# Kernel optimization log

Hardware: AMD Instinct MI355X
Metric: run time of the kernel (lower is better)

The kernel has to match this reference:

```python
import jax, jax.numpy as jnp
import numpy as np

L = 8192   # residues / nodes
E = 524288 # contact-map edges (avg degree 64)
NEG_SLOPE = 0.2  # PyG GATConv default negative_slope


def gat_layer(x, src, dst, Wg, asrc, adst, bias):
    """PyG-style GATConv (v1), concat heads, eval mode (no dropout).
    x: [L, F_in]; Wg: [F_in, H*C]; asrc/adst: [H, C]; bias: [H*C]."""
    H, C = asrc.shape
    h = (x @ Wg).reshape(L, H, C)                      # [L,H,C]
    a_s = jnp.einsum('nhc,hc->nh', h, asrc)            # [L,H]
    a_d = jnp.einsum('nhc,hc->nh', h, adst)            # [L,H]
    e = jax.nn.leaky_relu(a_s[src] + a_d[dst], NEG_SLOPE)  # [E',H]
    # softmax over incoming edges of each destination node
    m = jax.ops.segment_max(e, dst, num_segments=L)
    ex = jnp.exp(e - m[dst])
    denom = jax.ops.segment_sum(ex, dst, num_segments=L)
    alpha = ex / (denom[dst] + 1e-16)                  # [E',H]
    msg = h[src] * alpha[:, :, None]                   # [E',H,C]
    out = jax.ops.segment_sum(msg, dst, num_segments=L)  # [L,H,C]
    return out.reshape(L, H * C) + bias


def setup_inputs() -> dict:
    key = jax.random.key(0)
    ks = jax.random.split(key, 16)
    def g(k, shape, scale=0.05):
        return (jax.random.normal(k, shape, dtype=jnp.float32) * scale)
    return {
        'input_seq': jax.random.normal(ks[0], (1, L, 26), dtype=jnp.float32),
        'edge_index': jax.random.randint(ks[1], (2, E), 0, L, dtype=jnp.int32),
        'W1': g(ks[2], (26, 1024)),
        'W2': g(ks[3], (1024, 256)),
        'Wg1': g(ks[4], (256, 256)),
        'asrc1': g(ks[5], (4, 64)),
        'adst1': g(ks[6], (4, 64)),
        'b1': g(ks[7], (256,)),
        'Wg2': g(ks[8], (256, 512)),
        'asrc2': g(ks[9], (4, 128)),
        'adst2': g(ks[10], (4, 128)),
        'b2': g(ks[11], (512,)),
        'fcW': g(ks[12], (512, 512)),
        'fcb': g(ks[13], (512,)),
        'outW': g(ks[14], (512, 489)),
        'outb': g(ks[15], (489,)),
    }


def reference(input_seq, edge_index, W1, W2, Wg1, asrc1, adst1, b1,
              Wg2, asrc2, adst2, b2, fcW, fcb, outW, outb):
    # input_layer: Linear(26,1024,no bias) -> ReLU -> Linear(1024,256,no bias)
    x = jax.nn.relu(input_seq[0] @ W1) @ W2            # [L,256]
    # add self-loops (PyG GATConv default)
    loops = jnp.arange(L, dtype=edge_index.dtype)
    src = jnp.concatenate([edge_index[0], loops])
    dst = jnp.concatenate([edge_index[1], loops])
    # two GAT layers with ReLU activation
    x = jax.nn.relu(gat_layer(x, src, dst, Wg1, asrc1, adst1, b1))  # [L,256]
    x = jax.nn.relu(gat_layer(x, src, dst, Wg2, asrc2, adst2, b2))  # [L,512]
    # sum-pool over residues (x.sum(dim=1) with batch=1)
    pooled = x.sum(axis=0, keepdims=True)              # [1,512]
    # fc layers (dropout inactive in eval)
    h = jax.nn.relu(pooled @ fcW + fcb)                # [1,512]
    return h @ outW + outb                             # [1,489]
```

## Files before the change

### kernel.cpp

```cpp
#include <hip/hip_runtime.h>
#include <hip/hip_bf16.h>

constexpr int L = 8192;
constexpr int H = 4;

typedef __attribute__((ext_vector_type(8))) short bf16x8;
typedef __attribute__((ext_vector_type(8))) unsigned short u16x8;
typedef __attribute__((ext_vector_type(4))) float f32x4;

#if defined(__has_builtin)
#  if __has_builtin(__builtin_amdgcn_fdot2_f32_bf16)
#    define HAVE_DOT2 1
#  endif
#endif
#ifndef HAVE_DOT2
#  define HAVE_DOT2 0
#endif
#if HAVE_DOT2
typedef __attribute__((ext_vector_type(2))) __bf16 bfx2;
#endif

static __device__ __forceinline__ float lrelu(float e) {
  return e > 0.f ? e : 0.2f * e;
}
static __device__ __forceinline__ float b2f(unsigned short s) {
  return __uint_as_float(((unsigned)s) << 16);
}
static __device__ __forceinline__ unsigned short f2b(float f) {
  __hip_bfloat16 h = __float2bfloat16(f);
  return *reinterpret_cast<unsigned short*>(&h);
}
static __device__ __forceinline__ float dot2a(unsigned hv, unsigned m, float acc) {
#if HAVE_DOT2
  return __builtin_amdgcn_fdot2_f32_bf16(
      __builtin_bit_cast(bfx2, hv), __builtin_bit_cast(bfx2, m), acc, false);
#else
  return acc + b2f((unsigned short)(hv & 0xffffu)) * b2f((unsigned short)(m & 0xffffu))
             + b2f((unsigned short)(hv >> 16)) * b2f((unsigned short)(m >> 16));
#endif
}

__global__ __launch_bounds__(256) void conv_combo(
    const float* __restrict__ seq, const float* __restrict__ W1,
    const float* __restrict__ W2, const float* __restrict__ Wg1,
    const float* __restrict__ Wg2, const float* __restrict__ fcW,
    const float* __restrict__ outW, const int* __restrict__ ei,
    const float* __restrict__ as1, const float* __restrict__ ad1,
    const float* __restrict__ as2, const float* __restrict__ ad2,
    int E, int Etot,
    __hip_bfloat16* __restrict__ xb, __hip_bfloat16* __restrict__ W1t,
    __hip_bfloat16* __restrict__ W2t, __hip_bfloat16* __restrict__ Wg1t,
    __hip_bfloat16* __restrict__ Wg2t, float* __restrict__ fcWt,
    float* __restrict__ outWt, float* __restrict__ wa2,
    int* __restrict__ deg, int* __restrict__ rank) {
  __shared__ float tile[32][33];
  int t = threadIdx.x;
  if (blockIdx.x < 992) {
    int b = blockIdx.x;
    const float* src; void* dst; bool obf16; int K, N, Kout, kt, nt;
    if (b < 256)               { src = W2;  dst = W2t;  obf16 = true;  K = 1024; N = 256; Kout = 1024; nt = b & 7;  kt = b >> 3; }
    else if ((b -= 256) < 64)  { src = Wg1; dst = Wg1t; obf16 = true;  K = 256;  N = 256; Kout = 256;  nt = b & 7;  kt = b >> 3; }
    else if ((b -= 64) < 128)  { src = Wg2; dst = Wg2t; obf16 = true;  K = 256;  N = 512; Kout = 256;  nt = b & 15; kt = b >> 4; }
    else if ((b -= 128) < 256) { src = fcW; dst = fcWt; obf16 = false; K = 512;  N = 512; Kout = 512;  nt = b & 15; kt = b >> 4; }
    else if ((b -= 256) < 256) { src = outW;dst = outWt;obf16 = false; K = 512;  N = 489; Kout = 512;  nt = b & 15; kt = b >> 4; }
    else { b -= 256;             src = W1;  dst = W1t;  obf16 = true;  K = 26;   N = 1024;Kout = 32;   nt = b;      kt = 0; }
    int lr = t >> 3, lc4 = (t & 7) * 4;
    int gk = kt * 32 + lr, gn = nt * 32 + lc4;
    float4 v = {0.f, 0.f, 0.f, 0.f};
    if (gk < K) {
      const float* p = &src[(size_t)gk * N + gn];
      v.x = (gn + 0 < N) ? p[0] : 0.f;
      v.y = (gn + 1 < N) ? p[1] : 0.f;
      v.z = (gn + 2 < N) ? p[2] : 0.f;
      v.w = (gn + 3 < N) ? p[3] : 0.f;
    }
    tile[lr][lc4 + 0] = v.x; tile[lr][lc4 + 1] = v.y;
    tile[lr][lc4 + 2] = v.z; tile[lr][lc4 + 3] = v.w;
    __syncthreads();
    int on = nt * 32 + lr, ok = kt * 32 + lc4;
    if (on >= N || ok >= Kout) return;
    float o0 = tile[lc4 + 0][lr], o1 = tile[lc4 + 1][lr];
    float o2 = tile[lc4 + 2][lr], o3 = tile[lc4 + 3][lr];
    if (obf16) {
      ushort4 u = {f2b(o0), f2b(o1), f2b(o2), f2b(o3)};
      *(ushort4*)&((__hip_bfloat16*)dst)[(size_t)on * Kout + ok] = u;
    } else {
      float4 u = {o0, o1, o2, o3};
      *(float4*)&((float*)dst)[(size_t)on * Kout + ok] = u;
    }
    return;
  }
  int bb = blockIdx.x - 992;
  if (bb < 1024) {
    int i = bb * 256 + t;
    int r = i >> 5, k = i & 31;
    xb[i] = __float2bfloat16(k < 26 ? seq[r * 26 + k] : 0.f);
    return;
  }
  bb -= 1024;
  int lane = t & 63, wid = t >> 6;
  if (bb < 512) {
    int idx = bb * 4 + wid;
    int k = idx >> 3, o = idx & 7, h = o & 3;
    const float* av = (o < 4) ? as1 : ad1;
    float v = Wg1[k * 256 + h * 64 + lane] * av[h * 64 + lane];
#pragma unroll
    for (int off = 32; off > 0; off >>= 1) v += __shfl_xor(v, off);
    if (lane == 0) Wg1t[(size_t)(256 + o) * 256 + k] = __float2bfloat16(v);
    return;
  }
  bb -= 512;
  if (bb < 512) {
    int idx = bb * 4 + wid;
    int k = idx >> 3, o = idx & 7, h = o & 3;
    const float* av = (o < 4) ? as2 : ad2;
    float v = Wg2[k * 512 + h * 128 + lane] * av[h * 128 + lane]
            + Wg2[k * 512 + h * 128 + 64 + lane] * av[h * 128 + 64 + lane];
#pragma unroll
    for (int off = 32; off > 0; off >>= 1) v += __shfl_xor(v, off);
    if (lane == 0) wa2[idx] = v;
    return;
  }
  bb -= 512;
  if (bb < 56) {
    int i = bb * 256 + t;
    ((__hip_bfloat16*)Wg1t)[(size_t)264 * 256 + i] = __float2bfloat16(0.f);
    return;
  }
  bb -= 56;
  int e = bb * 256 + t;
  if (e < Etot) {
    int dst = (e < E) ? ei[E + e] : (e - E);
    rank[e] = atomicAdd(&deg[dst], 1);
  }
}

template<int BK, bool RELU, bool ASD>
__global__ __launch_bounds__(256) void gemm_big(
    const __hip_bfloat16* __restrict__ A, const __hip_bfloat16* __restrict__ Bt,
    __hip_bfloat16* __restrict__ C, float* __restrict__ asd,
    int M, int N, int K) {
  __shared__ __align__(16) short As[128][BK + 8];
  __shared__ __align__(16) short Bs[64][BK + 8];
  int tid = threadIdx.x;
  int m0 = blockIdx.y * 128, n0 = blockIdx.x * 64;
  int w = tid >> 6, lane = tid & 63;
  int wm = (w >> 1) * 64, wn = (w & 1) * 32;
  f32x4 acc[4][2] = {};
  for (int k0 = 0; k0 < K; k0 += BK) {
    if constexpr (BK == 64) {
#pragma unroll
      for (int i = 0; i < 4; i++) {
        int ch = i * 256 + tid; int r = ch >> 3, kg = ch & 7;
        *(bf16x8*)&As[r][kg * 8] = *(const bf16x8*)&A[(size_t)(m0 + r) * K + k0 + kg * 8];
      }
#pragma unroll
      for (int i = 0; i < 2; i++) {
        int ch = i * 256 + tid; int r = ch >> 3, kg = ch & 7;
        *(bf16x8*)&Bs[r][kg * 8] = *(const bf16x8*)&Bt[(size_t)(n0 + r) * K + k0 + kg * 8];
      }
    } else {
#pragma unroll
      for (int i = 0; i < 2; i++) {
        int ch = i * 256 + tid; int r = ch >> 2, kg = ch & 3;
        *(bf16x8*)&As[r][kg * 8] = *(const bf16x8*)&A[(size_t)(m0 + r) * K + k0 + kg * 8];
      }
      { int r = tid >> 2, kg = tid & 3;
        *(bf16x8*)&Bs[r][kg * 8] = *(const bf16x8*)&Bt[(size_t)(n0 + r) * K + k0 + kg * 8]; }
    }
    __syncthreads();
    int kk = (lane >> 4) * 8;
#pragma unroll
    for (int ks = 0; ks < BK / 32; ks++) {
      bf16x8 af[4], bfr[2];
#pragma unroll
      for (int m = 0; m < 4; m++)
        af[m] = *(const bf16x8*)&As[wm + m * 16 + (lane & 15)][ks * 32 + kk];
#pragma unroll
      for (int n = 0; n < 2; n++)
        bfr[n] = *(const bf16x8*)&Bs[wn + n * 16 + (lane & 15)][ks * 32 + kk];
#pragma unroll
      for (int m = 0; m < 4; m++)
#pragma unroll
        for (int n = 0; n < 2; n++)
          acc[m][n] = __builtin_amdgcn_mfma_f32_16x16x32_bf16(af[m], bfr[n], acc[m][n], 0, 0, 0);
    }
    __syncthreads();
  }
#pragma unroll
  for (int m = 0; m < 4; m++) {
#pragma unroll
    for (int n = 0; n < 2; n++) {
      int col = n0 + wn + n * 16 + (lane & 15);
#pragma unroll
      for (int j = 0; j < 4; j++) {
        int row = m0 + wm + m * 16 + (lane >> 4) * 4 + j;
        float v = acc[m][n][j];
        if (RELU) v = fmaxf(v, 0.f);
        if (!ASD) {
          C[(size_t)row * N + col] = __float2bfloat16(v);
        } else {
          if (col < N) C[(size_t)row * N + col] = __float2bfloat16(v);
          else if (col < N + 8) asd[(size_t)row * 8 + (col - N)] = v;
        }
      }
    }
  }
}

__global__ __launch_bounds__(256) void gemm_head(
    const __hip_bfloat16* __restrict__ agg,
    const __hip_bfloat16* __restrict__ Wg2t,
    const float* __restrict__ b2,
    float* __restrict__ pooled) {
  constexpr int BK = 64;
  __shared__ __align__(16) short As[128][BK + 8];
  __shared__ __align__(16) short Bs[64][BK + 8];
  __shared__ float s_cs[4][32];
  int tid = threadIdx.x;
  int z = blockIdx.z;
  int m0 = blockIdx.y * 128, n0 = blockIdx.x * 64;
  const __hip_bfloat16* A = agg + (size_t)z * 256;
  const __hip_bfloat16* Bt = Wg2t + (size_t)z * 128 * 256;
  int w = tid >> 6, lane = tid & 63;
  int wm = (w >> 1) * 64, wn = (w & 1) * 32;
  f32x4 acc[4][2] = {};
  for (int k0 = 0; k0 < 256; k0 += BK) {
#pragma unroll
    for (int i = 0; i < 4; i++) {
      int ch = i * 256 + tid; int r = ch >> 3, kg = ch & 7;
      *(bf16x8*)&As[r][kg * 8] = *(const bf16x8*)&A[(size_t)(m0 + r) * 1024 + k0 + kg * 8];
    }
#pragma unroll
    for (int i = 0; i < 2; i++) {
      int ch = i * 256 + tid; int r = ch >> 3, kg = ch & 7;
      *(bf16x8*)&Bs[r][kg * 8] = *(const bf16x8*)&Bt[(size_t)(n0 + r) * 256 + k0 + kg * 8];
    }
    __syncthreads();
    int kk = (lane >> 4) * 8;
#pragma unroll
    for (int ks = 0; ks < BK / 32; ks++) {
      bf16x8 af[4], bfr[2];
#pragma unroll
      for (int m = 0; m < 4; m++)
        af[m] = *(const bf16x8*)&As[wm + m * 16 + (lane & 15)][ks * 32 + kk];
#pragma unroll
      for (int n = 0; n < 2; n++)
        bfr[n] = *(const bf16x8*)&Bs[wn + n * 16 + (lane & 15)][ks * 32 + kk];
#pragma unroll
      for (int m = 0; m < 4; m++)
#pragma unroll
        for (int n = 0; n < 2; n++)
          acc[m][n] = __builtin_amdgcn_mfma_f32_16x16x32_bf16(af[m], bfr[n], acc[m][n], 0, 0, 0);
    }
    __syncthreads();
  }
  float cs[2] = {0.f, 0.f};
#pragma unroll
  for (int n = 0; n < 2; n++) {
    float bv = b2[z * 128 + n0 + wn + n * 16 + (lane & 15)];
#pragma unroll
    for (int m = 0; m < 4; m++)
#pragma unroll
      for (int j = 0; j < 4; j++)
        cs[n] += fmaxf(acc[m][n][j] + bv, 0.f);
  }
#pragma unroll
  for (int n = 0; n < 2; n++) {
    cs[n] += __shfl_xor(cs[n], 16);
    cs[n] += __shfl_xor(cs[n], 32);
  }
  if (lane < 16) { s_cs[w][lane] = cs[0]; s_cs[w][16 + lane] = cs[1]; }
  __syncthreads();
  if (tid < 64) {
    int c = tid;
    int bsel = c >> 5;
    float s = s_cs[bsel][c & 31] + s_cs[bsel + 2][c & 31];
    atomicAdd(&pooled[z * 128 + n0 + c], s);
  }
}

__global__ __launch_bounds__(1024) void scan_deg(const int* __restrict__ deg,
                                                 int* __restrict__ row_start,
                                                 float* __restrict__ pooled) {
  __shared__ int wsum[16];
  int t = threadIdx.x;
  if (t < 512) pooled[t] = 0.f;
  int lane = t & 63, w = t >> 6;
  int local[8];
  int sum = 0;
#pragma unroll
  for (int j = 0; j < 8; j++) { local[j] = deg[t * 8 + j]; sum += local[j]; }
  int v = sum;
#pragma unroll
  for (int off = 1; off < 64; off <<= 1) {
    int u = __shfl_up(v, off);
    if (lane >= off) v += u;
  }
  if (lane == 63) wsum[w] = v;
  __syncthreads();
  int woff = 0;
  for (int i = 0; i < w; i++) woff += wsum[i];
  int base = woff + v - sum;
#pragma unroll
  for (int j = 0; j < 8; j++) { row_start[t * 8 + j] = base; base += local[j]; }
  if (t == 1023) row_start[L] = base;
}

__global__ void scatter_edges(const int* __restrict__ ei, int E, int Etot,
                              const int* __restrict__ row_start,
                              const int* __restrict__ rank, int* __restrict__ csr_src) {
  int e = blockIdx.x * blockDim.x + threadIdx.x;
  if (e >= Etot) return;
  int srcv, dstv;
  if (e < E) { srcv = ei[e]; dstv = ei[E + e]; } else { srcv = dstv = e - E; }
  csr_src[row_start[dstv] + rank[e]] = srcv;
}

template<int C, bool ASD2>
__global__ __launch_bounds__(128) void gat_fused(
    const __hip_bfloat16* __restrict__ hfeat, const float* __restrict__ a_sd,
    const int* __restrict__ row_start, const int* __restrict__ csr_src,
    const float* __restrict__ bias, __hip_bfloat16* __restrict__ out,
    const float* __restrict__ wa2, float* __restrict__ a_sd2) {
  constexpr int HC = 4 * C;
  constexpr int VEC = HC / 64;
  constexpr int BATCH = 12;
  int wid = threadIdx.x >> 6, lane = threadIdx.x & 63;
  int n = blockIdx.x * 2 + wid;
  int c0 = lane * VEC;
  int hl = (c0 / C) & 3;
  int rs = row_start[n], re = row_start[n + 1];
  float4 ad4 = *(const float4*)&a_sd[(size_t)n * 8 + 4];

  float dp[4] = {0.f, 0.f, 0.f, 0.f};
  float acc[VEC] = {};
  const unsigned short* hbase = (const unsigned short*)hfeat;
  bool sel32 = (lane & 32) != 0;
  bool sel16 = (lane & 16) != 0;

  int base = rs;
  int cnt = min(64, re - rs);
  int srcv = 0;
  float4 as4 = {0.f, 0.f, 0.f, 0.f};
  if (lane < cnt) {
    srcv = csr_src[rs + lane];
    as4 = *(const float4*)&a_sd[(size_t)srcv * 8];
  }

  while (base < re) {
    float w0 = 0.f, w1 = 0.f, w2 = 0.f, w3 = 0.f;
    if (lane < cnt) {
      w0 = __expf(lrelu(as4.x + ad4.x));
      w1 = __expf(lrelu(as4.y + ad4.y));
      w2 = __expf(lrelu(as4.z + ad4.z));
      w3 = __expf(lrelu(as4.w + ad4.w));
    }
    dp[0] += w0; dp[1] += w1; dp[2] += w2; dp[3] += w3;
    unsigned pk01 = (unsigned)f2b(w0) | ((unsigned)f2b(w1) << 16);
    unsigned pk23 = (unsigned)f2b(w2) | ((unsigned)f2b(w3) << 16);
    int cur_src = srcv;
    unsigned cur_p01 = pk01, cur_p23 = pk23;
    int cur_cnt = cnt;
    int nbase = base + 64;
    bool have_next = nbase < re;
    cnt = min(64, re - nbase);
    srcv = 0;
    if (have_next && lane < cnt) srcv = csr_src[nbase + lane];
    float4 nas4 = {0.f, 0.f, 0.f, 0.f};
    bool did_asd = false;

    auto consume_edge = [&](int sr, unsigned p01, unsigned p23,
                            unsigned h0, unsigned h1v) {
      unsigned word = sel32 ? p23 : p01;
      unsigned tsel = sel16 ? (word >> 16) : (word & 0xffffu);
      unsigned mlo = tsel, mhi = tsel << 16;
      acc[0] = dot2a(h0, mlo, acc[0]);
      acc[1] = dot2a(h0, mhi, acc[1]);
      acc[2] = dot2a(h1v, mlo, acc[2]);
      acc[3] = dot2a(h1v, mhi, acc[3]);
    };

    int j = 0;
    for (; j + BATCH <= cur_cnt; j += BATCH) {
      int srs[BATCH];
#pragma unroll
      for (int k = 0; k < BATCH; k++) srs[k] = __builtin_amdgcn_readlane(cur_src, j + k);
      uint2 hv[BATCH];
#pragma unroll
      for (int k = 0; k < BATCH; k++)
        hv[k] = *(const uint2*)&hbase[(size_t)srs[k] * HC + c0];
      if (j == 0 && have_next) {
        if (lane < cnt) nas4 = *(const float4*)&a_sd[(size_t)srcv * 8];
        did_asd = true;
      }
#pragma unroll
      for (int k = 0; k < BATCH; k++) {
        unsigned p01 = (unsigned)__builtin_amdgcn_readlane((int)cur_p01, j + k);
        unsigned p23 = (unsigned)__builtin_amdgcn_readlane((int)cur_p23, j + k);
        consume_edge(srs[k], p01, p23, hv[k].x, hv[k].y);
      }
    }
    if (have_next && !did_asd && lane < cnt)
      nas4 = *(const float4*)&a_sd[(size_t)srcv * 8];
    for (; j < cur_cnt; j++) {
      int sr = __builtin_amdgcn_readlane(cur_src, j);
      uint2 hvv = *(const uint2*)&hbase[(size_t)sr * HC + c0];
      unsigned p01 = (unsigned)__builtin_amdgcn_readlane((int)cur_p01, j);
      unsigned p23 = (unsigned)__builtin_amdgcn_readlane((int)cur_p23, j);
      consume_edge(sr, p01, p23, hvv.x, hvv.y);
    }
    as4 = nas4;
    base = nbase;
  }

#pragma unroll
  for (int off = 32; off > 0; off >>= 1) {
#pragma unroll
    for (int h = 0; h < 4; h++) dp[h] += __shfl_xor(dp[h], off);
  }
  float dsel = hl == 0 ? dp[0] : hl == 1 ? dp[1] : hl == 2 ? dp[2] : dp[3];
  float inv = 1.f / (dsel + 1e-16f);

#pragma unroll
  for (int k = 0; k < VEC; k++)
    acc[k] = fmaxf(fmaf(acc[k], inv, bias[c0 + k]), 0.f);
  unsigned short* op = (unsigned short*)out + (size_t)n * HC + c0;
  ushort4 ov = {f2b(acc[0]), f2b(acc[1]), f2b(acc[2]), f2b(acc[3])};
  *(ushort4*)op = ov;

  if constexpr (ASD2) {
    float p[8] = {};
#pragma unroll
    for (int q = 0; q < VEC; q++) {
      const float* wr = &wa2[(size_t)(c0 + q) * 8];
#pragma unroll
      for (int o = 0; o < 8; o++) p[o] = fmaf(acc[q], wr[o], p[o]);
    }
#pragma unroll
    for (int off = 32; off > 0; off >>= 1) {
#pragma unroll
      for (int o = 0; o < 8; o++) p[o] += __shfl_xor(p[o], off);
    }
    if (lane == 0) {
      float4 p0 = {p[0], p[1], p[2], p[3]};
      float4 p1 = {p[4], p[5], p[6], p[7]};
      *(float4*)&a_sd2[(size_t)n * 8 + 0] = p0;
      *(float4*)&a_sd2[(size_t)n * 8 + 4] = p1;
    }
  }
}

__global__ __launch_bounds__(128) void gat_agg(
    const __hip_bfloat16* __restrict__ feat,
    const float* __restrict__ a_sd,
    const int* __restrict__ row_start, const int* __restrict__ csr_src,
    __hip_bfloat16* __restrict__ agg) {
  constexpr int BATCH = 8;
  int wid = threadIdx.x >> 6, lane = threadIdx.x & 63;
  int n = blockIdx.x * 2 + wid;
  int c0 = lane * 4;
  int rs = row_start[n], re = row_start[n + 1];
  float4 ad4 = *(const float4*)&a_sd[(size_t)n * 8 + 4];

  float dp[4] = {0.f, 0.f, 0.f, 0.f};
  float acc[4][4] = {};
  const unsigned short* hbase = (const unsigned short*)feat;

  int base = rs;
  int cnt = min(64, re - rs);
  int srcv = 0;
  float4 as4 = {0.f, 0.f, 0.f, 0.f};
  if (lane < cnt) {
    srcv = csr_src[rs + lane];
    as4 = *(const float4*)&a_sd[(size_t)srcv * 8];
  }

  while (base < re) {
    float w0 = 0.f, w1 = 0.f, w2 = 0.f, w3 = 0.f;
    if (lane < cnt) {
      w0 = __expf(lrelu(as4.x + ad4.x));
      w1 = __expf(lrelu(as4.y + ad4.y));
      w2 = __expf(lrelu(as4.z + ad4.z));
      w3 = __expf(lrelu(as4.w + ad4.w));
    }
    dp[0] += w0; dp[1] += w1; dp[2] += w2; dp[3] += w3;
    unsigned pk01 = (unsigned)f2b(w0) | ((unsigned)f2b(w1) << 16);
    unsigned pk23 = (unsigned)f2b(w2) | ((unsigned)f2b(w3) << 16);
    int cur_src = srcv;
    unsigned cur_p01 = pk01, cur_p23 = pk23;
    int cur_cnt = cnt;
    int nbase = base + 64;
    bool have_next = nbase < re;
    cnt = min(64, re - nbase);
    srcv = 0;
    if (have_next && lane < cnt) srcv = csr_src[nbase + lane];
    float4 nas4 = {0.f, 0.f, 0.f, 0.f};
    bool did_asd = false;

    auto consume_edge = [&](unsigned p01, unsigned p23, unsigned hx, unsigned hy) {
      unsigned m0lo = p01 & 0xffffu,      m0hi = p01 << 16;
      unsigned m1lo = p01 >> 16,          m1hi = p01 & 0xffff0000u;
      unsigned m2lo = p23 & 0xffffu,      m2hi = p23 << 16;
      unsigned m3lo = p23 >> 16,          m3hi = p23 & 0xffff0000u;
      acc[0][0] = dot2a(hx, m0lo, acc[0][0]); acc[0][1] = dot2a(hx, m0hi, acc[0][1]);
      acc[0][2] = dot2a(hy, m0lo, acc[0][2]); acc[0][3] = dot2a(hy, m0hi, acc[0][3]);
      acc[1][0] = dot2a(hx, m1lo, acc[1][0]); acc[1][1] = dot2a(hx, m1hi, acc[1][1]);
      acc[1][2] = dot2a(hy, m1lo, acc[1][2]); acc[1][3] = dot2a(hy, m1hi, acc[1][3]);
      acc[2][0] = dot2a(hx, m2lo, acc[2][0]); acc[2][1] = dot2a(hx, m2hi, acc[2][1]);
      acc[2][2] = dot2a(hy, m2lo, acc[2][2]); acc[2][3] = dot2a(hy, m2hi, acc[2][3]);
      acc[3][0] = dot2a(hx, m3lo, acc[3][0]); acc[3][1] = dot2a(hx, m3hi, acc[3][1]);
      acc[3][2] = dot2a(hy, m3lo, acc[3][2]); acc[3][3] = dot2a(hy, m3hi, acc[3][3]);
    };

    int j = 0;
    for (; j + BATCH <= cur_cnt; j += BATCH) {
      int srs[BATCH];
#pragma unroll
      for (int k = 0; k < BATCH; k++) srs[k] = __builtin_amdgcn_readlane(cur_src, j + k);
      uint2 hv[BATCH];
#pragma unroll
      for (int k = 0; k < BATCH; k++)
        hv[k] = *(const uint2*)&hbase[(size_t)srs[k] * 256 + c0];
      if (j == 0 && have_next) {
        if (lane < cnt) nas4 = *(const float4*)&a_sd[(size_t)srcv * 8];
        did_asd = true;
      }
#pragma unroll
      for (int k = 0; k < BATCH; k++) {
        unsigned p01 = (unsigned)__builtin_amdgcn_readlane((int)cur_p01, j + k);
        unsigned p23 = (unsigned)__builtin_amdgcn_readlane((int)cur_p23, j + k);
        consume_edge(p01, p23, hv[k].x, hv[k].y);
      }
    }
    if (have_next && !did_asd && lane < cnt)
      nas4 = *(const float4*)&a_sd[(size_t)srcv * 8];
    for (; j < cur_cnt; j++) {
      int sr = __builtin_amdgcn_readlane(cur_src, j);
      uint2 hvv = *(const uint2*)&hbase[(size_t)sr * 256 + c0];
      unsigned p01 = (unsigned)__builtin_amdgcn_readlane((int)cur_p01, j);
      unsigned p23 = (unsigned)__builtin_amdgcn_readlane((int)cur_p23, j);
      consume_edge(p01, p23, hvv.x, hvv.y);
    }
    as4 = nas4;
    base = nbase;
  }

#pragma unroll
  for (int off = 32; off > 0; off >>= 1) {
#pragma unroll
    for (int h = 0; h < 4; h++) dp[h] += __shfl_xor(dp[h], off);
  }
  unsigned short* op = (unsigned short*)agg + (size_t)n * 1024 + c0;
#pragma unroll
  for (int h = 0; h < 4; h++) {
    float inv = 1.f / (dp[h] + 1e-16f);
    ushort4 ov = {f2b(acc[h][0] * inv), f2b(acc[h][1] * inv),
                  f2b(acc[h][2] * inv), f2b(acc[h][3] * inv)};
    *(ushort4*)(op + h * 256) = ov;
  }
}

__global__ __launch_bounds__(256) void fc1(const float* __restrict__ pooled,
                                           const float* __restrict__ Wt,
                                           const float* __restrict__ b,
                                           float* __restrict__ out) {
  __shared__ float pv[512];
  __shared__ float red[256];
  int t = threadIdx.x;
  pv[t] = pooled[t]; pv[t + 256] = pooled[t + 256];
  __syncthreads();
  int ol = t >> 4;
  int o = blockIdx.x * 16 + ol;
  int ks = (t & 15) * 32;
  float p = 0.f;
  const float* wr = &Wt[(size_t)o * 512 + ks];
#pragma unroll
  for (int kk = 0; kk < 32; kk++) p = fmaf(pv[ks + kk], wr[kk], p);
  red[t] = p;
  __syncthreads();
  if ((t & 15) == 0) {
    float s2 = 0.f;
#pragma unroll
    for (int i = 0; i < 16; i++) s2 += red[ol * 16 + i];
    out[o] = fmaxf(s2 + b[o], 0.f);
  }
}

__global__ __launch_bounds__(256) void fc2(const float* __restrict__ h,
                                           const float* __restrict__ Wt,
                                           const float* __restrict__ outb,
                                           float* __restrict__ out) {
  __shared__ float pv[512];
  __shared__ float red[256];
  int t = threadIdx.x;
  pv[t] = h[t]; pv[t + 256] = h[t + 256];
  __syncthreads();
  int ol = t >> 4;
  int o = blockIdx.x * 16 + ol;
  int ks = (t & 15) * 32;
  float p = 0.f;
  const float* wr = &Wt[(size_t)o * 512 + ks];
#pragma unroll
  for (int kk = 0; kk < 32; kk++) p = fmaf(pv[ks + kk], wr[kk], p);
  red[t] = p;
  __syncthreads();
  if ((t & 15) == 0 && o < 489) {
    float s2 = 0.f;
#pragma unroll
    for (int i = 0; i < 16; i++) s2 += red[ol * 16 + i];
    out[o] = s2 + outb[o];
  }
}

extern "C" void kernel_launch(void* const* d_in, const int* in_sizes, int n_in,
                              void* d_out, int out_size, void* d_ws, size_t ws_size,
                              hipStream_t stream) {
  const float* seq   = (const float*)d_in[0];
  const int*   ei    = (const int*)d_in[1];
  const float* W1    = (const float*)d_in[2];
  const float* W2    = (const float*)d_in[3];
  const float* Wg1   = (const float*)d_in[4];
  const float* asrc1 = (const float*)d_in[5];
  const float* adst1 = (const float*)d_in[6];
  const float* b1    = (const float*)d_in[7];
  const float* Wg2   = (const float*)d_in[8];
  const float* asrc2 = (const float*)d_in[9];
  const float* adst2 = (const float*)d_in[10];
  const float* b2    = (const float*)d_in[11];
  const float* fcW   = (const float*)d_in[12];
  const float* fcb   = (const float*)d_in[13];
  const float* outW  = (const float*)d_in[14];
  const float* outb  = (const float*)d_in[15];
  float* outp = (float*)d_out;

  const int E = in_sizes[1] / 2;
  const int Etot = E + L;

  char* ws = (char*)d_ws;
  __hip_bfloat16* mlp1 = (__hip_bfloat16*)(ws + 0);
  __hip_bfloat16* agg2 = (__hip_bfloat16*)(ws + 0);
  __hip_bfloat16* x0   = (__hip_bfloat16*)(ws + (24u << 20));
  __hip_bfloat16* h1   = (__hip_bfloat16*)(ws + (28u << 20));
  __hip_bfloat16* out1 = (__hip_bfloat16*)(ws + (32u << 20));
  size_t off = (36u << 20);
  __hip_bfloat16* xb   = (__hip_bfloat16*)(ws + off); off += (size_t)L * 32 * 2;
  __hip_bfloat16* W1t  = (__hip_bfloat16*)(ws + off); off += (size_t)1024 * 32 * 2;
  __hip_bfloat16* W2t  = (__hip_bfloat16*)(ws + off); off += (size_t)256 * 1024 * 2;
  __hip_bfloat16* Wg1t = (__hip_bfloat16*)(ws + off); off += (size_t)320 * 256 * 2;
  __hip_bfloat16* Wg2t = (__hip_bfloat16*)(ws + off); off += (size_t)512 * 256 * 2;
  float* fcWt  = (float*)(ws + off); off += (size_t)512 * 512 * 4;
  float* outWt = (float*)(ws + off); off += (size_t)512 * 512 * 4;
  int* csr_src = (int*)(ws + off); off += (size_t)Etot * 4;
  int* rank    = (int*)(ws + off); off += (size_t)Etot * 4;
  off = (off + 255) & ~(size_t)255;
  int* row_start = (int*)(ws + off); off += (size_t)(L + 1) * 4;
  off = (off + 255) & ~(size_t)255;
  int* deg    = (int*)(ws + off); off += (size_t)L * 4;
  float* a_sd1 = (float*)(ws + off); off += (size_t)L * 8 * 4;
  float* a_sd2 = (float*)(ws + off); off += (size_t)L * 8 * 4;
  float* wa2 = (float*)(ws + off); off += 2048 * 4;
  float* pooled = (float*)(ws + off); off += 512 * 4;
  float* hbuf   = (float*)(ws + off); off += 512 * 4;

  hipMemsetAsync(deg, 0, (size_t)L * 4, stream);

  int tailB = 1024 + 512 + 512 + 56 + (Etot + 255) / 256;
  conv_combo<<<992 + tailB, 256, 0, stream>>>(
      seq, W1, W2, Wg1, Wg2, fcW, outW, ei, asrc1, adst1, asrc2, adst2, E, Etot,
      xb, W1t, W2t, Wg1t, Wg2t, fcWt, outWt, wa2, deg, rank);

  scan_deg<<<1, 1024, 0, stream>>>(deg, row_start, pooled);
  scatter_edges<<<(Etot + 255) / 256, 256, 0, stream>>>(ei, E, Etot, row_start, rank, csr_src);

  gemm_big<32, true, false><<<dim3(16, 64), 256, 0, stream>>>(xb, W1t, mlp1, nullptr, L, 1024, 32);
  gemm_big<64, false, false><<<dim3(4, 64), 256, 0, stream>>>(mlp1, W2t, x0, nullptr, L, 256, 1024);

  gemm_big<64, false, true><<<dim3(5, 64), 256, 0, stream>>>(x0, Wg1t, h1, a_sd1, L, 256, 256);
  gat_fused<64, true><<<4096, 128, 0, stream>>>(h1, a_sd1, row_start, csr_src, b1, out1, wa2, a_sd2);

  gat_agg<<<4096, 128, 0, stream>>>(out1, a_sd2, row_start, csr_src, agg2);
  gemm_head<<<dim3(2, 64, 4), 256, 0, stream>>>(agg2, Wg2t, b2, pooled);

  fc1<<<32, 256, 0, stream>>>(pooled, fcWt, fcb, hbuf);
  fc2<<<31, 256, 0, stream>>>(hbuf, outWt, outb, outp);
}
```

Before: 183.6 us.

## Process two destination nodes per wavefront with interleaved gather pipelines in GAT kernels

Both GAT aggregation kernels now assign two destination nodes to each wavefront and interleave their neighbor gathers. While one node's batch of eight feature rows is being consumed, the next batch for that node is issued, so the two nodes' loads and dot-product work overlap. This is meant to hide the latency of the random row gathers by keeping more loads in flight per wave, and the grid is halved to match. In exchange, each wave holds twice the accumulators and buffers, which raises register pressure and may lower occupancy; the gat_fused batch size also drops from twelve to eight.

```diff
diff --git a/kernel.cpp b/kernel.cpp
--- a/kernel.cpp
+++ b/kernel.cpp
@@ -324,129 +324,175 @@
     const float* __restrict__ bias, __hip_bfloat16* __restrict__ out,
     const float* __restrict__ wa2, float* __restrict__ a_sd2) {
   constexpr int HC = 4 * C;
-  constexpr int VEC = HC / 64;
-  constexpr int BATCH = 12;
+  constexpr int B = 8;
   int wid = threadIdx.x >> 6, lane = threadIdx.x & 63;
-  int n = blockIdx.x * 2 + wid;
-  int c0 = lane * VEC;
-  int hl = (c0 / C) & 3;
-  int rs = row_start[n], re = row_start[n + 1];
-  float4 ad4 = *(const float4*)&a_sd[(size_t)n * 8 + 4];
-
-  float dp[4] = {0.f, 0.f, 0.f, 0.f};
-  float acc[VEC] = {};
+  int nA = blockIdx.x * 4 + wid * 2, nB = nA + 1;
+  int c0 = lane * 4;
+  bool sel32 = (lane & 32) != 0, sel16 = (lane & 16) != 0;
+  int hl = lane >> 4;
   const unsigned short* hbase = (const unsigned short*)hfeat;
-  bool sel32 = (lane & 32) != 0;
-  bool sel16 = (lane & 16) != 0;
-
-  int base = rs;
-  int cnt = min(64, re - rs);
-  int srcv = 0;
-  float4 as4 = {0.f, 0.f, 0.f, 0.f};
-  if (lane < cnt) {
-    srcv = csr_src[rs + lane];
-    as4 = *(const float4*)&a_sd[(size_t)srcv * 8];
-  }
-
-  while (base < re) {
-    float w0 = 0.f, w1 = 0.f, w2 = 0.f, w3 = 0.f;
-    if (lane < cnt) {
-      w0 = __expf(lrelu(as4.x + ad4.x));
-      w1 = __expf(lrelu(as4.y + ad4.y));
-      w2 = __expf(lrelu(as4.z + ad4.z));
-      w3 = __expf(lrelu(as4.w + ad4.w));
-    }
-    dp[0] += w0; dp[1] += w1; dp[2] += w2; dp[3] += w3;
-    unsigned pk01 = (unsigned)f2b(w0) | ((unsigned)f2b(w1) << 16);
-    unsigned pk23 = (unsigned)f2b(w2) | ((unsigned)f2b(w3) << 16);
-    int cur_src = srcv;
-    unsigned cur_p01 = pk01, cur_p23 = pk23;
-    int cur_cnt = cnt;
-    int nbase = base + 64;
-    bool have_next = nbase < re;
-    cnt = min(64, re - nbase);
-    srcv = 0;
-    if (have_next && lane < cnt) srcv = csr_src[nbase + lane];
-    float4 nas4 = {0.f, 0.f, 0.f, 0.f};
-    bool did_asd = false;
-
-    auto consume_edge = [&](int sr, unsigned p01, unsigned p23,
-                            unsigned h0, unsigned h1v) {
-      unsigned word = sel32 ? p23 : p01;
-      unsigned tsel = sel16 ? (word >> 16) : (word & 0xffffu);
-      unsigned mlo = tsel, mhi = tsel << 16;
-      acc[0] = dot2a(h0, mlo, acc[0]);
-      acc[1] = dot2a(h0, mhi, acc[1]);
-      acc[2] = dot2a(h1v, mlo, acc[2]);
-      acc[3] = dot2a(h1v, mhi, acc[3]);
+
+  int rsA = row_start[nA], reA = row_start[nA + 1];
+  int rsB = row_start[nB], reB = row_start[nB + 1];
+  float4 adA = *(const float4*)&a_sd[(size_t)nA * 8 + 4];
+  float4 adB = *(const float4*)&a_sd[(size_t)nB * 8 + 4];
+  float dpA[4] = {}, dpB[4] = {};
+  float accA[4] = {}, accB[4] = {};
+
+  int baseA = rsA, baseB = rsB;
+  int cntA = min(64, reA - rsA), cntB = min(64, reB - rsB);
+  int srcA = 0, srcB = 0;
+  float4 asA = {0.f,0.f,0.f,0.f}, asB = {0.f,0.f,0.f,0.f};
+  if (lane < cntA) { srcA = csr_src[rsA + lane]; asA = *(const float4*)&a_sd[(size_t)srcA * 8]; }
+  if (lane < cntB) { srcB = csr_src[rsB + lane]; asB = *(const float4*)&a_sd[(size_t)srcB * 8]; }
+
+  auto edge4 = [&](float* acc, unsigned p01, unsigned p23, uint2 hv) {
+    unsigned word = sel32 ? p23 : p01;
+    unsigned tsel = sel16 ? (word >> 16) : (word & 0xffffu);
+    acc[0] = dot2a(hv.x, tsel, acc[0]);
+    acc[1] = dot2a(hv.x, tsel << 16, acc[1]);
+    acc[2] = dot2a(hv.y, tsel, acc[2]);
+    acc[3] = dot2a(hv.y, tsel << 16, acc[3]);
+  };
+
+  while (baseA < reA || baseB < reB) {
+    bool actA = baseA < reA, actB = baseB < reB;
+    int ccA = actA ? cntA : 0, ccB = actB ? cntB : 0;
+    unsigned pA01 = 0, pA23 = 0, pB01 = 0, pB23 = 0;
+    if (actA) {
+      float w0=0.f,w1=0.f,w2=0.f,w3=0.f;
+      if (lane < ccA) {
+        w0 = __expf(lrelu(asA.x + adA.x)); w1 = __expf(lrelu(asA.y + adA.y));
+        w2 = __expf(lrelu(asA.z + adA.z)); w3 = __expf(lrelu(asA.w + adA.w));
+      }
+      dpA[0]+=w0; dpA[1]+=w1; dpA[2]+=w2; dpA[3]+=w3;
+      pA01 = (unsigned)f2b(w0) | ((unsigned)f2b(w1) << 16);
+      pA23 = (unsigned)f2b(w2) | ((unsigned)f2b(w3) << 16);
+    }
+    if (actB) {
+      float w0=0.f,w1=0.f,w2=0.f,w3=0.f;
+      if (lane < ccB) {
+        w0 = __expf(lrelu(asB.x + adB.x)); w1 = __expf(lrelu(asB.y + adB.y));
+        w2 = __expf(lrelu(asB.z + adB.z)); w3 = __expf(lrelu(asB.w + adB.w));
+      }
+      dpB[0]+=w0; dpB[1]+=w1; dpB[2]+=w2; dpB[3]+=w3;
+      pB01 = (unsigned)f2b(w0) | ((unsigned)f2b(w1) << 16);
+      pB23 = (unsigned)f2b(w2) | ((unsigned)f2b(w3) << 16);
+    }
+    int curSA = srcA, curSB = srcB;
+    int nbA = baseA + 64, nbB = baseB + 64;
+    bool hnA = actA && nbA < reA, hnB = actB && nbB < reB;
+    int ncA = min(64, reA - nbA), ncB = min(64, reB - nbB);
+    srcA = 0; srcB = 0;
+    if (hnA && lane < ncA) srcA = csr_src[nbA + lane];
+    if (hnB && lane < ncB) srcB = csr_src[nbB + lane];
+
+    uint2 hvA[B], hvB[B];
+    auto issueA = [&](int j) {
+#pragma unroll
+      for (int k = 0; k < B; k++) {
+        int sr = __builtin_amdgcn_readlane(curSA, j + k);
+        hvA[k] = *(const uint2*)&hbase[(size_t)sr * HC + c0];
+      }
     };
-
-    int j = 0;
-    for (; j + BATCH <= cur_cnt; j += BATCH) {
-      int srs[BATCH];
-#pragma unroll
-      for (int k = 0; k < BATCH; k++) srs[k] = __builtin_amdgcn_readlane(cur_src, j + k);
-      uint2 hv[BATCH];
-#pragma unroll
-      for (int k = 0; k < BATCH; k++)
-        hv[k] = *(const uint2*)&hbase[(size_t)srs[k] * HC + c0];
-      if (j == 0 && have_next) {
-        if (lane < cnt) nas4 = *(const float4*)&a_sd[(size_t)srcv * 8];
-        did_asd = true;
-      }
-#pragma unroll
-      for (int k = 0; k < BATCH; k++) {
-        unsigned p01 = (unsigned)__builtin_amdgcn_readlane((int)cur_p01, j + k);
-        unsigned p23 = (unsigned)__builtin_amdgcn_readlane((int)cur_p23, j + k);
-        consume_edge(srs[k], p01, p23, hv[k].x, hv[k].y);
-      }
-    }
-    if (have_next && !did_asd && lane < cnt)
-      nas4 = *(const float4*)&a_sd[(size_t)srcv * 8];
-    for (; j < cur_cnt; j++) {
-      int sr = __builtin_amdgcn_readlane(cur_src, j);
-      uint2 hvv = *(const uint2*)&hbase[(size_t)sr * HC + c0];
-      unsigned p01 = (unsigned)__builtin_amdgcn_readlane((int)cur_p01, j);
-      unsigned p23 = (unsigned)__builtin_amdgcn_readlane((int)cur_p23, j);
-      consume_edge(sr, p01, p23, hvv.x, hvv.y);
-    }
-    as4 = nas4;
-    base = nbase;
+    auto issueB = [&](int j) {
+#pragma unroll
+      for (int k = 0; k < B; k++) {
+        int sr = __builtin_amdgcn_readlane(curSB, j + k);
+        hvB[k] = *(const uint2*)&hbase[(size_t)sr * HC + c0];
+      }
+    };
+    int jA = 0, jB = 0;
+    bool pendA = (B <= ccA), pendB = (B <= ccB);
+    if (pendA) issueA(0);
+    if (pendB) issueB(0);
+    float4 nasA = {0.f,0.f,0.f,0.f}, nasB = {0.f,0.f,0.f,0.f};
+    if (hnA && lane < ncA) nasA = *(const float4*)&a_sd[(size_t)srcA * 8];
+    if (hnB && lane < ncB) nasB = *(const float4*)&a_sd[(size_t)srcB * 8];
+
+    while (pendA || pendB) {
+      if (pendA) {
+#pragma unroll
+        for (int k = 0; k < B; k++) {
+          unsigned p01 = (unsigned)__builtin_amdgcn_readlane((int)pA01, jA + k);
+          unsigned p23 = (unsigned)__builtin_amdgcn_readlane((int)pA23, jA + k);
+          edge4(accA, p01, p23, hvA[k]);
+        }
+        jA += B;
+        pendA = (jA + B <= ccA);
+        if (pendA) issueA(jA);
+      }
+      if (pendB) {
+#pragma unroll
+        for (int k = 0; k < B; k++) {
+          unsigned p01 = (unsigned)__builtin_amdgcn_readlane((int)pB01, jB + k);
+          unsigned p23 = (unsigned)__builtin_amdgcn_readlane((int)pB23, jB + k);
+          edge4(accB, p01, p23, hvB[k]);
+        }
+        jB += B;
+        pendB = (jB + B <= ccB);
+        if (pendB) issueB(jB);
+      }
+    }
+    for (; jA < ccA; jA++) {
+      int sr = __builtin_amdgcn_readlane(curSA, jA);
+      uint2 hv = *(const uint2*)&hbase[(size_t)sr * HC + c0];
+      unsigned p01 = (unsigned)__builtin_amdgcn_readlane((int)pA01, jA);
+      unsigned p23 = (unsigned)__builtin_amdgcn_readlane((int)pA23, jA);
+      edge4(accA, p01, p23, hv);
+    }
+    for (; jB < ccB; jB++) {
+      int sr = __builtin_amdgcn_readlane(curSB, jB);
+      uint2 hv = *(const uint2*)&hbase[(size_t)sr * HC + c0];
+      unsigned p01 = (unsigned)__builtin_amdgcn_readlane((int)pB01, jB);
+      unsigned p23 = (unsigned)__builtin_amdgcn_readlane((int)pB23, jB);
+      edge4(accB, p01, p23, hv);
+    }
+    if (actA) { asA = nasA; baseA = nbA; cntA = ncA; }
+    if (actB) { asB = nasB; baseB = nbB; cntB = ncB; }
   }
 
 #pragma unroll
   for (int off = 32; off > 0; off >>= 1) {
 #pragma unroll
-    for (int h = 0; h < 4; h++) dp[h] += __shfl_xor(dp[h], off);
-  }
-  float dsel = hl == 0 ? dp[0] : hl == 1 ? dp[1] : hl == 2 ? dp[2] : dp[3];
-  float inv = 1.f / (dsel + 1e-16f);
-
-#pragma unroll
-  for (int k = 0; k < VEC; k++)
-    acc[k] = fmaxf(fmaf(acc[k], inv, bias[c0 + k]), 0.f);
-  unsigned short* op = (unsigned short*)out + (size_t)n * HC + c0;
-  ushort4 ov = {f2b(acc[0]), f2b(acc[1]), f2b(acc[2]), f2b(acc[3])};
-  *(ushort4*)op = ov;
+    for (int h = 0; h < 4; h++) { dpA[h] += __shfl_xor(dpA[h], off); dpB[h] += __shfl_xor(dpB[h], off); }
+  }
+  float dselA = hl == 0 ? dpA[0] : hl == 1 ? dpA[1] : hl == 2 ? dpA[2] : dpA[3];
+  float dselB = hl == 0 ? dpB[0] : hl == 1 ? dpB[1] : hl == 2 ? dpB[2] : dpB[3];
+  float invA = 1.f / (dselA + 1e-16f), invB = 1.f / (dselB + 1e-16f);
+#pragma unroll
+  for (int k = 0; k < 4; k++) {
+    accA[k] = fmaxf(fmaf(accA[k], invA, bias[c0 + k]), 0.f);
+    accB[k] = fmaxf(fmaf(accB[k], invB, bias[c0 + k]), 0.f);
+  }
+  ushort4 ovA = {f2b(accA[0]), f2b(accA[1]), f2b(accA[2]), f2b(accA[3])};
+  ushort4 ovB = {f2b(accB[0]), f2b(accB[1]), f2b(accB[2]), f2b(accB[3])};
+  *(ushort4*)((unsigned short*)out + (size_t)nA * HC + c0) = ovA;
+  *(ushort4*)((unsigned short*)out + (size_t)nB * HC + c0) = ovB;
 
   if constexpr (ASD2) {
-    float p[8] = {};
-#pragma unroll
-    for (int q = 0; q < VEC; q++) {
+    float pA[8] = {}, pB[8] = {};
+#pragma unroll
+    for (int q = 0; q < 4; q++) {
       const float* wr = &wa2[(size_t)(c0 + q) * 8];
 #pragma unroll
-      for (int o = 0; o < 8; o++) p[o] = fmaf(acc[q], wr[o], p[o]);
+      for (int o = 0; o < 8; o++) {
+        pA[o] = fmaf(accA[q], wr[o], pA[o]);
+        pB[o] = fmaf(accB[q], wr[o], pB[o]);
+      }
     }
 #pragma unroll
     for (int off = 32; off > 0; off >>= 1) {
 #pragma unroll
-      for (int o = 0; o < 8; o++) p[o] += __shfl_xor(p[o], off);
+      for (int o = 0; o < 8; o++) { pA[o] += __shfl_xor(pA[o], off); pB[o] += __shfl_xor(pB[o], off); }
     }
     if (lane == 0) {
-      float4 p0 = {p[0], p[1], p[2], p[3]};
-      float4 p1 = {p[4], p[5], p[6], p[7]};
-      *(float4*)&a_sd2[(size_t)n * 8 + 0] = p0;
-      *(float4*)&a_sd2[(size_t)n * 8 + 4] = p1;
+      float4 a0 = {pA[0], pA[1], pA[2], pA[3]}, a1 = {pA[4], pA[5], pA[6], pA[7]};
+      float4 b0 = {pB[0], pB[1], pB[2], pB[3]}, b1 = {pB[4], pB[5], pB[6], pB[7]};
+      *(float4*)&a_sd2[(size_t)nA * 8 + 0] = a0;
+      *(float4*)&a_sd2[(size_t)nA * 8 + 4] = a1;
+      *(float4*)&a_sd2[(size_t)nB * 8 + 0] = b0;
+      *(float4*)&a_sd2[(size_t)nB * 8 + 4] = b1;
     }
   }
 }
@@ -456,108 +502,155 @@
     const float* __restrict__ a_sd,
     const int* __restrict__ row_start, const int* __restrict__ csr_src,
     __hip_bfloat16* __restrict__ agg) {
-  constexpr int BATCH = 8;
+  constexpr int B = 8;
   int wid = threadIdx.x >> 6, lane = threadIdx.x & 63;
-  int n = blockIdx.x * 2 + wid;
+  int nA = blockIdx.x * 4 + wid * 2, nB = nA + 1;
   int c0 = lane * 4;
-  int rs = row_start[n], re = row_start[n + 1];
-  float4 ad4 = *(const float4*)&a_sd[(size_t)n * 8 + 4];
-
-  float dp[4] = {0.f, 0.f, 0.f, 0.f};
-  float acc[4][4] = {};
   const unsigned short* hbase = (const unsigned short*)feat;
 
-  int base = rs;
-  int cnt = min(64, re - rs);
-  int srcv = 0;
-  float4 as4 = {0.f, 0.f, 0.f, 0.f};
-  if (lane < cnt) {
-    srcv = csr_src[rs + lane];
-    as4 = *(const float4*)&a_sd[(size_t)srcv * 8];
-  }
-
-  while (base < re) {
-    float w0 = 0.f, w1 = 0.f, w2 = 0.f, w3 = 0.f;
-    if (lane < cnt) {
-      w0 = __expf(lrelu(as4.x + ad4.x));
-      w1 = __expf(lrelu(as4.y + ad4.y));
-      w2 = __expf(lrelu(as4.z + ad4.z));
-      w3 = __expf(lrelu(as4.w + ad4.w));
-    }
-    dp[0] += w0; dp[1] += w1; dp[2] += w2; dp[3] += w3;
-    unsigned pk01 = (unsigned)f2b(w0) | ((unsigned)f2b(w1) << 16);
-    unsigned pk23 = (unsigned)f2b(w2) | ((unsigned)f2b(w3) << 16);
-    int cur_src = srcv;
-    unsigned cur_p01 = pk01, cur_p23 = pk23;
-    int cur_cnt = cnt;
-    int nbase = base + 64;
-    bool have_next = nbase < re;
-    cnt = min(64, re - nbase);
-    srcv = 0;
-    if (have_next && lane < cnt) srcv = csr_src[nbase + lane];
-    float4 nas4 = {0.f, 0.f, 0.f, 0.f};
-    bool did_asd = false;
-
-    auto consume_edge = [&](unsigned p01, unsigned p23, unsigned hx, unsigned hy) {
-      unsigned m0lo = p01 & 0xffffu,      m0hi = p01 << 16;
-      unsigned m1lo = p01 >> 16,          m1hi = p01 & 0xffff0000u;
-      unsigned m2lo = p23 & 0xffffu,      m2hi = p23 << 16;
-      unsigned m3lo = p23 >> 16,          m3hi = p23 & 0xffff0000u;
-      acc[0][0] = dot2a(hx, m0lo, acc[0][0]); acc[0][1] = dot2a(hx, m0hi, acc[0][1]);
-      acc[0][2] = dot2a(hy, m0lo, acc[0][2]); acc[0][3] = dot2a(hy, m0hi, acc[0][3]);
-      acc[1][0] = dot2a(hx, m1lo, acc[1][0]); acc[1][1] = dot2a(hx, m1hi, acc[1][1]);
-      acc[1][2] = dot2a(hy, m1lo, acc[1][2]); acc[1][3] = dot2a(hy, m1hi, acc[1][3]);
-      acc[2][0] = dot2a(hx, m2lo, acc[2][0]); acc[2][1] = dot2a(hx, m2hi, acc[2][1]);
-      acc[2][2] = dot2a(hy, m2lo, acc[2][2]); acc[2][3] = dot2a(hy, m2hi, acc[2][3]);
-      acc[3][0] = dot2a(hx, m3lo, acc[3][0]); acc[3][1] = dot2a(hx, m3hi, acc[3][1]);
-      acc[3][2] = dot2a(hy, m3lo, acc[3][2]); acc[3][3] = dot2a(hy, m3hi, acc[3][3]);
+  int rsA = row_start[nA], reA = row_start[nA + 1];
+  int rsB = row_start[nB], reB = row_start[nB + 1];
+  float4 adA = *(const float4*)&a_sd[(size_t)nA * 8 + 4];
+  float4 adB = *(const float4*)&a_sd[(size_t)nB * 8 + 4];
+  float dpA[4] = {}, dpB[4] = {};
+  float accA[4][4] = {}, accB[4][4] = {};
+
+  int baseA = rsA, baseB = rsB;
+  int cntA = min(64, reA - rsA), cntB = min(64, reB - rsB);
+  int srcA = 0, srcB = 0;
+  float4 asA = {0.f,0.f,0.f,0.f}, asB = {0.f,0.f,0.f,0.f};
+  if (lane < cntA) { srcA = csr_src[rsA + lane]; asA = *(const float4*)&a_sd[(size_t)srcA * 8]; }
+  if (lane < cntB) { srcB = csr_src[rsB + lane]; asB = *(const float4*)&a_sd[(size_t)srcB * 8]; }
+
+  auto edge16 = [&](float (*acc)[4], unsigned p01, unsigned p23, uint2 hv) {
+    unsigned m0lo = p01 & 0xffffu,      m0hi = p01 << 16;
+    unsigned m1lo = p01 >> 16,          m1hi = p01 & 0xffff0000u;
+    unsigned m2lo = p23 & 0xffffu,      m2hi = p23 << 16;
+    unsigned m3lo = p23 >> 16,          m3hi = p23 & 0xffff0000u;
+    acc[0][0] = dot2a(hv.x, m0lo, acc[0][0]); acc[0][1] = dot2a(hv.x, m0hi, acc[0][1]);
+    acc[0][2] = dot2a(hv.y, m0lo, acc[0][2]); acc[0][3] = dot2a(hv.y, m0hi, acc[0][3]);
+    acc[1][0] = dot2a(hv.x, m1lo, acc[1][0]); acc[1][1] = dot2a(hv.x, m1hi, acc[1][1]);
+    acc[1][2] = dot2a(hv.y, m1lo, acc[1][2]); acc[1][3] = dot2a(hv.y, m1hi, acc[1][3]);
+    acc[2][0] = dot2a(hv.x, m2lo, acc[2][0]); acc[2][1] = dot2a(hv.x, m2hi, acc[2][1]);
+    acc[2][2] = dot2a(hv.y, m2lo, acc[2][2]); acc[2][3] = dot2a(hv.y, m2hi, acc[2][3]);
+    acc[3][0] = dot2a(hv.x, m3lo, acc[3][0]); acc[3][1] = dot2a(hv.x, m3hi, acc[3][1]);
+    acc[3][2] = dot2a(hv.y, m3lo, acc[3][2]); acc[3][3] = dot2a(hv.y, m3hi, acc[3][3]);
+  };
+
+  while (baseA < reA || baseB < reB) {
+    bool actA = baseA < reA, actB = baseB < reB;
+    int ccA = actA ? cntA : 0, ccB = actB ? cntB : 0;
+    unsigned pA01 = 0, pA23 = 0, pB01 = 0, pB23 = 0;
+    if (actA) {
+      float w0=0.f,w1=0.f,w2=0.f,w3=0.f;
+      if (lane < ccA) {
+        w0 = __expf(lrelu(asA.x + adA.x)); w1 = __expf(lrelu(asA.y + adA.y));
+        w2 = __expf(lrelu(asA.z + adA.z)); w3 = __expf(lrelu(asA.w + adA.w));
+      }
+      dpA[0]+=w0; dpA[1]+=w1; dpA[2]+=w2; dpA[3]+=w3;
+      pA01 = (unsigned)f2b(w0) | ((unsigned)f2b(w1) << 16);
+      pA23 = (unsigned)f2b(w2) | ((unsigned)f2b(w3) << 16);
+    }
+    if (actB) {
+      float w0=0.f,w1=0.f,w2=0.f,w3=0.f;
+      if (lane < ccB) {
+        w0 = __expf(lrelu(asB.x + adB.x)); w1 = __expf(lrelu(asB.y + adB.y));
+        w2 = __expf(lrelu(asB.z + adB.z)); w3 = __expf(lrelu(asB.w + adB.w));
+      }
+      dpB[0]+=w0; dpB[1]+=w1; dpB[2]+=w2; dpB[3]+=w3;
+      pB01 = (unsigned)f2b(w0) | ((unsigned)f2b(w1) << 16);
+      pB23 = (unsigned)f2b(w2) | ((unsigned)f2b(w3) << 16);
+    }
+    int curSA = srcA, curSB = srcB;
+    int nbA = baseA + 64, nbB = baseB + 64;
+    bool hnA = actA && nbA < reA, hnB = actB && nbB < reB;
+    int ncA = min(64, reA - nbA), ncB = min(64, reB - nbB);
+    srcA = 0; srcB = 0;
+    if (hnA && lane < ncA) srcA = csr_src[nbA + lane];
+    if (hnB && lane < ncB) srcB = csr_src[nbB + lane];
+
+    uint2 hvA[B], hvB[B];
+    auto issueA = [&](int j) {
+#pragma unroll
+      for (int k = 0; k < B; k++) {
+        int sr = __builtin_amdgcn_readlane(curSA, j + k);
+        hvA[k] = *(const uint2*)&hbase[(size_t)sr * 256 + c0];
+      }
     };
-
-    int j = 0;
-    for (; j + BATCH <= cur_cnt; j += BATCH) {
-      int srs[BATCH];
-#pragma unroll
-      for (int k = 0; k < BATCH; k++) srs[k] = __builtin_amdgcn_readlane(cur_src, j + k);
-      uint2 hv[BATCH];
-#pragma unroll
-      for (int k = 0; k < BATCH; k++)
-        hv[k] = *(const uint2*)&hbase[(size_t)srs[k] * 256 + c0];
-      if (j == 0 && have_next) {
-        if (lane < cnt) nas4 = *(const float4*)&a_sd[(size_t)srcv * 8];
-        did_asd = true;
-      }
-#pragma unroll
-      for (int k = 0; k < BATCH; k++) {
-        unsigned p01 = (unsigned)__builtin_amdgcn_readlane((int)cur_p01, j + k);
-        unsigned p23 = (unsigned)__builtin_amdgcn_readlane((int)cur_p23, j + k);
-        consume_edge(p01, p23, hv[k].x, hv[k].y);
-      }
-    }
-    if (have_next && !did_asd && lane < cnt)
-      nas4 = *(const float4*)&a_sd[(size_t)srcv * 8];
-    for (; j < cur_cnt; j++) {
-      int sr = __builtin_amdgcn_readlane(cur_src, j);
-      uint2 hvv = *(const uint2*)&hbase[(size_t)sr * 256 + c0];
-      unsigned p01 = (unsigned)__builtin_amdgcn_readlane((int)cur_p01, j);
-      unsigned p23 = (unsigned)__builtin_amdgcn_readlane((int)cur_p23, j);
-      consume_edge(p01, p23, hvv.x, hvv.y);
-    }
-    as4 = nas4;
-    base = nbase;
+    auto issueB = [&](int j) {
+#pragma unroll
+      for (int k = 0; k < B; k++) {
+        int sr = __builtin_amdgcn_readlane(curSB, j + k);
+        hvB[k] = *(const uint2*)&hbase[(size_t)sr * 256 + c0];
+      }
+    };
+    int jA = 0, jB = 0;
+    bool pendA = (B <= ccA), pendB = (B <= ccB);
+    if (pendA) issueA(0);
+    if (pendB) issueB(0);
+    float4 nasA = {0.f,0.f,0.f,0.f}, nasB = {0.f,0.f,0.f,0.f};
+    if (hnA && lane < ncA) nasA = *(const float4*)&a_sd[(size_t)srcA * 8];
+    if (hnB && lane < ncB) nasB = *(const float4*)&a_sd[(size_t)srcB * 8];
+
+    while (pendA || pendB) {
+      if (pendA) {
+#pragma unroll
+        for (int k = 0; k < B; k++) {
+          unsigned p01 = (unsigned)__builtin_amdgcn_readlane((int)pA01, jA + k);
+          unsigned p23 = (unsigned)__builtin_amdgcn_readlane((int)pA23, jA + k);
+          edge16(accA, p01, p23, hvA[k]);
+        }
+        jA += B;
+        pendA = (jA + B <= ccA);
+        if (pendA) issueA(jA);
+      }
+      if (pendB) {
+#pragma unroll
+        for (int k = 0; k < B; k++) {
+          unsigned p01 = (unsigned)__builtin_amdgcn_readlane((int)pB01, jB + k);
+          unsigned p23 = (unsigned)__builtin_amdgcn_readlane((int)pB23, jB + k);
+          edge16(accB, p01, p23, hvB[k]);
+        }
+        jB += B;
+        pendB = (jB + B <= ccB);
+        if (pendB) issueB(jB);
+      }
+    }
+    for (; jA < ccA; jA++) {
+      int sr = __builtin_amdgcn_readlane(curSA, jA);
+      uint2 hv = *(const uint2*)&hbase[(size_t)sr * 256 + c0];
+      unsigned p01 = (unsigned)__builtin_amdgcn_readlane((int)pA01, jA);
+      unsigned p23 = (unsigned)__builtin_amdgcn_readlane((int)pA23, jA);
+      edge16(accA, p01, p23, hv);
+    }
+    for (; jB < ccB; jB++) {
+      int sr = __builtin_amdgcn_readlane(curSB, jB);
+      uint2 hv = *(const uint2*)&hbase[(size_t)sr * 256 + c0];
+      unsigned p01 = (unsigned)__builtin_amdgcn_readlane((int)pB01, jB);
+      unsigned p23 = (unsigned)__builtin_amdgcn_readlane((int)pB23, jB);
+      edge16(accB, p01, p23, hv);
+    }
+    if (actA) { asA = nasA; baseA = nbA; cntA = ncA; }
+    if (actB) { asB = nasB; baseB = nbB; cntB = ncB; }
   }
 
 #pragma unroll
   for (int off = 32; off > 0; off >>= 1) {
 #pragma unroll
-    for (int h = 0; h < 4; h++) dp[h] += __shfl_xor(dp[h], off);
-  }
-  unsigned short* op = (unsigned short*)agg + (size_t)n * 1024 + c0;
+    for (int h = 0; h < 4; h++) { dpA[h] += __shfl_xor(dpA[h], off); dpB[h] += __shfl_xor(dpB[h], off); }
+  }
+  unsigned short* opA = (unsigned short*)agg + (size_t)nA * 1024 + c0;
+  unsigned short* opB = (unsigned short*)agg + (size_t)nB * 1024 + c0;
 #pragma unroll
   for (int h = 0; h < 4; h++) {
-    float inv = 1.f / (dp[h] + 1e-16f);
-    ushort4 ov = {f2b(acc[h][0] * inv), f2b(acc[h][1] * inv),
-                  f2b(acc[h][2] * inv), f2b(acc[h][3] * inv)};
-    *(ushort4*)(op + h * 256) = ov;
+    float ivA = 1.f / (dpA[h] + 1e-16f);
+    float ivB = 1.f / (dpB[h] + 1e-16f);
+    ushort4 oA = {f2b(accA[h][0] * ivA), f2b(accA[h][1] * ivA),
+                  f2b(accA[h][2] * ivA), f2b(accA[h][3] * ivA)};
+    ushort4 oB = {f2b(accB[h][0] * ivB), f2b(accB[h][1] * ivB),
+                  f2b(accB[h][2] * ivB), f2b(accB[h][3] * ivB)};
+    *(ushort4*)(opA + h * 256) = oA;
+    *(ushort4*)(opB + h * 256) = oB;
   }
 }
 
@@ -677,9 +770,9 @@
   gemm_big<64, false, false><<<dim3(4, 64), 256, 0, stream>>>(mlp1, W2t, x0, nullptr, L, 256, 1024);
 
   gemm_big<64, false, true><<<dim3(5, 64), 256, 0, stream>>>(x0, Wg1t, h1, a_sd1, L, 256, 256);
-  gat_fused<64, true><<<4096, 128, 0, stream>>>(h1, a_sd1, row_start, csr_src, b1, out1, wa2, a_sd2);
-
-  gat_agg<<<4096, 128, 0, stream>>>(out1, a_sd2, row_start, csr_src, agg2);
+  gat_fused<64, true><<<2048, 128, 0, stream>>>(h1, a_sd1, row_start, csr_src, b1, out1, wa2, a_sd2);
+
+  gat_agg<<<2048, 128, 0, stream>>>(out1, a_sd2, row_start, csr_src, agg2);
   gemm_head<<<dim3(2, 64, 4), 256, 0, stream>>>(agg2, Wg2t, b2, pooled);
 
   fc1<<<32, 256, 0, stream>>>(pooled, fcWt, fcb, hbuf);
```

Result: slower. 199.4 us (+8.6%).
